# Optimization experiments

Hardware: AMD Instinct MI355X
Metric: run time of the kernel (lower is better)

The kernel has to match this reference:

```python
import jax, jax.numpy as jnp
import numpy as np
import math

B, NT, NS, NPS, D, H = 32, 64, 256, 256, 768, 12
DH = D // H
KEEP_RATIO = 0.7
LENS_KEEP = math.ceil(KEEP_RATIO * NS)  # 180
EPS = 1e-5


def _ln(z, g, b):
    m = jnp.mean(z, axis=-1, keepdims=True)
    v = jnp.mean((z - m) ** 2, axis=-1, keepdims=True)
    return (z - m) * jax.lax.rsqrt(v + EPS) * g + b


def setup_inputs() -> dict:
    key = jax.random.key(0)
    ks = jax.random.split(key, 12)
    p = lambda i, shape: jax.random.normal(ks[i], shape, jnp.float32) * 0.02
    return {
        'x': jax.random.normal(ks[0], (B, NT + NS, D), jnp.float32),
        'ps': jax.random.normal(ks[1], (B, NPS, D), jnp.float32),
        'global_index_template': jnp.broadcast_to(jnp.arange(NT, dtype=jnp.int32), (B, NT)),
        'global_index_search': jnp.broadcast_to(jnp.arange(NS, dtype=jnp.int32), (B, NS)),
        'g1': jnp.ones((D,), jnp.float32), 'b1': jnp.zeros((D,), jnp.float32),
        'Wqkv': p(2, (D, 3 * D)),
        'Wproj': p(3, (D, D)), 'bproj': jnp.zeros((D,), jnp.float32),
        'gt': jnp.ones((D,), jnp.float32), 'bt': jnp.zeros((D,), jnp.float32),
        'Wq': p(4, (D, D)), 'Wk': p(5, (D, D)), 'Wv': p(6, (D, D)),
        'Wtp': p(7, (D, D)), 'btp': jnp.zeros((D,), jnp.float32),
        'g2': jnp.ones((D,), jnp.float32), 'b2': jnp.zeros((D,), jnp.float32),
        'W1': p(8, (D, 4 * D)), 'b1m': jnp.zeros((4 * D,), jnp.float32),
        'W2': p(9, (4 * D, D)), 'b2m': jnp.zeros((D,), jnp.float32),
    }


def reference(x, ps, global_index_template, global_index_search,
              g1, b1, Wqkv, Wproj, bproj, gt, bt, Wq, Wk, Wv, Wtp, btp,
              g2, b2, W1, b1m, W2, b2m):
    scale = DH ** -0.5
    N = NT + NS
    # --- self attention over [template; search] tokens, raw attn exposed ---
    h = _ln(x, g1, b1)
    qkv = (h @ Wqkv).reshape(B, N, 3, H, DH)
    q = qkv[:, :, 0].transpose(0, 2, 1, 3)  # [B,H,N,DH]
    k = qkv[:, :, 1].transpose(0, 2, 1, 3)
    v = qkv[:, :, 2].transpose(0, 2, 1, 3)
    attn = jax.nn.softmax(jnp.einsum('bhqd,bhkd->bhqk', q, k) * scale, axis=-1)
    xa = jnp.einsum('bhqk,bhkd->bqhd', attn, v).reshape(B, N, D)
    x = x + xa @ Wproj + bproj

    # --- candidate elimination: keep top LENS_KEEP search tokens by
    # template->search attention averaged over heads and template queries ---
    attn_t = attn[:, :, :NT, NT:].mean(axis=(1, 2))  # [B, NS]
    order = jnp.argsort(-attn_t, axis=1)             # descending
    topk_idx = order[:, :LENS_KEEP]
    non_topk_idx = order[:, LENS_KEEP:]
    keep_index = jnp.take_along_axis(global_index_search, topk_idx, axis=1)
    removed_index = jnp.take_along_axis(global_index_search, non_topk_idx, axis=1)
    tokens_s = jnp.take_along_axis(x[:, NT:], topk_idx[:, :, None], axis=1)  # [B,LENS_KEEP,D]
    x = jnp.concatenate([x[:, :NT], tokens_s], axis=1)  # [B, NT+LENS_KEEP, D]

    # --- temporal cross-attention: kept search tokens attend over ps ---
    s = x[:, NT:]
    sn = _ln(s, gt, bt)
    qT = (sn @ Wq).reshape(B, LENS_KEEP, H, DH).transpose(0, 2, 1, 3)
    kT = (ps @ Wk).reshape(B, NPS, H, DH).transpose(0, 2, 1, 3)
    vT = (ps @ Wv).reshape(B, NPS, H, DH).transpose(0, 2, 1, 3)
    attn2 = jax.nn.softmax(jnp.einsum('bhqd,bhkd->bhqk', qT, kT) * scale, axis=-1)
    sa = jnp.einsum('bhqk,bhkd->bqhd', attn2, vT).reshape(B, LENS_KEEP, D)
    s = s + sa @ Wtp + btp
    x = jnp.concatenate([x[:, :NT], s], axis=1)

    # --- MLP (exact GELU like torch default) ---
    h2 = _ln(x, g2, b2)
    x = x + jax.nn.gelu(h2 @ W1 + b1m, approximate=False) @ W2 + b2m

    return (x, global_index_template, keep_index, removed_index, attn)
```

## Files before the change

### kernel.cpp

```cpp
#include <hip/hip_runtime.h>
#include <hip/hip_bf16.h>

#define BB 32
#define NT 64
#define NS 256
#define NN 320
#define NPS 256
#define DD 768
#define HH 12
#define DHD 64
#define LK 180
#define NREM 76

#define OFF_HF    0LL
#define OFF_KF    7864320LL
#define OFF_QTF   15728640LL
#define OFF_QV    17301504LL
#define OFF_WQVT  25165824LL
#define OFF_XA    0LL
#define OFF_X1    12000000LL
#define OFF_X2    0LL
#define OFF_SN    6000000LL
#define OFF_QT2   20000000LL
#define OFF_KT    22300000LL
#define OFF_VT    25500000LL
#define OFF_SA    6000000LL
#define OFF_H2    12000000LL
#define OFF_MIDB  15000000LL
#define OFF_WTS2  29300000LL
#define OFF_ATP   30500000LL
#define OFF_TOPK  30600000LL
#define OFF_WSM   30700000LL

#define O_X    0LL
#define O_GIT  5996544LL
#define O_KEEP 5998592LL
#define O_REM  6004352LL
#define O_ATTN 6006784LL

typedef __attribute__((ext_vector_type(8))) short short8v;
typedef __attribute__((ext_vector_type(4))) float f32x4;

__device__ __forceinline__ float bf2f(unsigned short u) {
  return __uint_as_float((unsigned)u << 16);
}
__device__ __forceinline__ unsigned short f2bfu(float f) {
  __hip_bfloat16 h = __float2bfloat16(f);
  return *reinterpret_cast<unsigned short*>(&h);
}

template<int OMODE>
__global__ __launch_bounds__(256) void ln_kernel(
    const float* __restrict__ in, float* __restrict__ outf,
    unsigned short* __restrict__ outh,
    const float* __restrict__ g, const float* __restrict__ b,
    int rpb, long long bstride, int row0)
{
  int r = blockIdx.x, t = threadIdx.x;
  long long base = (long long)(r / rpb) * bstride + (long long)(r % rpb + row0) * DD;
  float v0 = in[base + t], v1 = in[base + 256 + t], v2 = in[base + 512 + t];
  __shared__ float red[256];
  red[t] = v0 + v1 + v2;
  __syncthreads();
  #pragma unroll
  for (int off = 128; off > 0; off >>= 1) { if (t < off) red[t] += red[t + off]; __syncthreads(); }
  float mean = red[0] * (1.f / 768.f);
  __syncthreads();
  float d0 = v0 - mean, d1 = v1 - mean, d2 = v2 - mean;
  red[t] = d0 * d0 + d1 * d1 + d2 * d2;
  __syncthreads();
  #pragma unroll
  for (int off = 128; off > 0; off >>= 1) { if (t < off) red[t] += red[t + off]; __syncthreads(); }
  float rstd = rsqrtf(red[0] * (1.f / 768.f) + 1e-5f);
  long long ob = (long long)r * DD;
  float o0 = d0 * rstd * g[t]       + b[t];
  float o1 = d1 * rstd * g[256 + t] + b[256 + t];
  float o2 = d2 * rstd * g[512 + t] + b[512 + t];
  if (OMODE == 0) {
    outf[ob + t] = o0; outf[ob + 256 + t] = o1; outf[ob + 512 + t] = o2;
  } else {
    outh[ob + t] = f2bfu(o0); outh[ob + 256 + t] = f2bfu(o1); outh[ob + 512 + t] = f2bfu(o2);
  }
}

__global__ __launch_bounds__(256) void cvt_wt(
    const float* __restrict__ W, unsigned short* __restrict__ Th,
    int K, int Nfull, int n0off, int zoff, long long zdststep)
{
  __shared__ float tile[32][33];
  int z = blockIdx.z;
  unsigned short* T = Th + (long long)z * zdststep;
  int ncol = n0off + z * zoff;
  int n0 = blockIdx.x * 32, k0 = blockIdx.y * 32;
  int tx = threadIdx.x & 31, ty4 = (threadIdx.x >> 5) * 4;
  #pragma unroll
  for (int i = 0; i < 4; ++i)
    tile[ty4 + i][tx] = W[(long long)(k0 + ty4 + i) * Nfull + ncol + n0 + tx];
  __syncthreads();
  #pragma unroll
  for (int i = 0; i < 4; ++i)
    T[(long long)(n0 + ty4 + i) * K + k0 + tx] = f2bfu(tile[tx][ty4 + i]);
}

__global__ __launch_bounds__(256) void cvt_w5(
    const float* __restrict__ Wa, const float* __restrict__ Wb,
    const float* __restrict__ Wc, const float* __restrict__ Wd,
    const float* __restrict__ We, unsigned short* __restrict__ Th)
{
  __shared__ float tile[32][33];
  const float* srcs[5] = {Wa, Wb, Wc, Wd, We};
  const float* W = srcs[blockIdx.z];
  unsigned short* T = Th + (long long)blockIdx.z * (768 * 768);
  int n0 = blockIdx.x * 32, k0 = blockIdx.y * 32;
  int tx = threadIdx.x & 31, ty4 = (threadIdx.x >> 5) * 4;
  #pragma unroll
  for (int i = 0; i < 4; ++i)
    tile[ty4 + i][tx] = W[(long long)(k0 + ty4 + i) * 768 + n0 + tx];
  __syncthreads();
  #pragma unroll
  for (int i = 0; i < 4; ++i)
    T[(long long)(n0 + ty4 + i) * 768 + k0 + tx] = f2bfu(tile[tx][ty4 + i]);
}

__global__ __launch_bounds__(512) void gemm_k(
    const float* __restrict__ A, int a_rpb, long long a_bstride,
    const float* __restrict__ W, int wst,
    float* __restrict__ Cf, int c_ld, int M, int K)
{
  __shared__ float As[16][132];
  __shared__ float Ws[16][132];
  int t = threadIdx.x;
  long long bm = (long long)blockIdx.y * 128;
  long long bn = (long long)blockIdx.x * 128;
  float acc[4][8] = {};
  int wid = t >> 6, lane = t & 63;
  int tm = (wid & 3) * 32 + (lane >> 3) * 4;
  int tn = (wid >> 2) * 64 + (lane & 7) * 8;
  int idx = t << 2;
  int am = idx >> 4, ak = idx & 15;
  int wk = idx >> 7, wn2 = idx & 127;
  long long r = bm + am;
  long long abase = (r / a_rpb) * a_bstride + (r % a_rpb) * (long long)K;
  for (int k0 = 0; k0 < K; k0 += 16) {
    const float4 a4 = *reinterpret_cast<const float4*>(A + abase + k0 + ak);
    As[ak + 0][am] = a4.x; As[ak + 1][am] = a4.y;
    As[ak + 2][am] = a4.z; As[ak + 3][am] = a4.w;
    *reinterpret_cast<float4*>(&Ws[wk][wn2]) =
        *reinterpret_cast<const float4*>(W + (long long)(k0 + wk) * wst + bn + wn2);
    __syncthreads();
    #pragma unroll
    for (int kk = 0; kk < 16; ++kk) {
      float a[4], w[8];
      *reinterpret_cast<float4*>(a)     = *reinterpret_cast<const float4*>(&As[kk][tm]);
      *reinterpret_cast<float4*>(w)     = *reinterpret_cast<const float4*>(&Ws[kk][tn]);
      *reinterpret_cast<float4*>(w + 4) = *reinterpret_cast<const float4*>(&Ws[kk][tn + 4]);
      #pragma unroll
      for (int i = 0; i < 4; ++i)
        #pragma unroll
        for (int j = 0; j < 8; ++j)
          acc[i][j] = fmaf(a[i], w[j], acc[i][j]);
    }
    __syncthreads();
  }
  #pragma unroll
  for (int i = 0; i < 4; ++i) {
    long long crow = (bm + tm + i) * c_ld;
    #pragma unroll
    for (int j = 0; j < 8; ++j)
      Cf[crow + bn + tn + j] = acc[i][j];
  }
}

template<int AF32>
__global__ __launch_bounds__(256) void gemm_mfma(
    const void* __restrict__ A, const unsigned short* __restrict__ Bt,
    const float* __restrict__ bias, const float* __restrict__ resid,
    float* __restrict__ Cf, int ldf,
    unsigned short* __restrict__ Cb, int ldb, int colsplit,
    int M, int N, int K,
    int c_rpb, long long c_bstride, int c_row0, int act)
{
  __shared__ unsigned short As[128 * 40], Bs[128 * 40];
  const unsigned short* Ab = (const unsigned short*)A;
  const float* Af = (const float*)A;
  int t = threadIdx.x;
  long long bm = (long long)blockIdx.y * 128;
  long long bn = (long long)blockIdx.x * 128;
  int wid = t >> 6, lane = t & 63;
  int wr = (wid >> 1) << 6, wc = (wid & 1) << 6;
  f32x4 acc[4][4];
  #pragma unroll
  for (int m = 0; m < 4; ++m)
    #pragma unroll
    for (int n = 0; n < 4; ++n) acc[m][n] = (f32x4){0.f, 0.f, 0.f, 0.f};
  for (int k0 = 0; k0 < K; k0 += 32) {
    #pragma unroll
    for (int l = 0; l < 2; ++l) {
      int e = (t + (l << 8)) << 3;
      int row = e >> 5, kk = e & 31;
      int ls = row * 40 + kk;
      if (AF32) {
        const float4 f0 = *reinterpret_cast<const float4*>(&Af[(bm + row) * K + k0 + kk]);
        const float4 f1 = *reinterpret_cast<const float4*>(&Af[(bm + row) * K + k0 + kk + 4]);
        ushort4 u0, u1;
        u0.x = f2bfu(f0.x); u0.y = f2bfu(f0.y); u0.z = f2bfu(f0.z); u0.w = f2bfu(f0.w);
        u1.x = f2bfu(f1.x); u1.y = f2bfu(f1.y); u1.z = f2bfu(f1.z); u1.w = f2bfu(f1.w);
        *reinterpret_cast<ushort4*>(&As[ls])     = u0;
        *reinterpret_cast<ushort4*>(&As[ls + 4]) = u1;
      } else {
        *reinterpret_cast<int4*>(&As[ls]) = *reinterpret_cast<const int4*>(&Ab[(bm + row) * K + k0 + kk]);
      }
      *reinterpret_cast<int4*>(&Bs[ls]) = *reinterpret_cast<const int4*>(&Bt[(bn + row) * K + k0 + kk]);
    }
    __syncthreads();
    int ra = (wr + (lane & 15)) * 40 + ((lane >> 4) << 3);
    int rb = (wc + (lane & 15)) * 40 + ((lane >> 4) << 3);
    short8v a[4], b[4];
    #pragma unroll
    for (int m = 0; m < 4; ++m) {
      a[m] = *reinterpret_cast<const short8v*>(&As[ra + m * 16 * 40]);
      b[m] = *reinterpret_cast<const short8v*>(&Bs[rb + m * 16 * 40]);
    }
    #pragma unroll
    for (int m = 0; m < 4; ++m)
      #pragma unroll
      for (int n = 0; n < 4; ++n)
        acc[m][n] = __builtin_amdgcn_mfma_f32_16x16x32_bf16(a[m], b[n], acc[m][n], 0, 0, 0);
    __syncthreads();
  }
  int ro = (lane >> 4) << 2, co = lane & 15;
  #pragma unroll
  for (int m = 0; m < 4; ++m) {
    #pragma unroll
    for (int j = 0; j < 4; ++j) {
      long long r = bm + wr + m * 16 + ro + j;
      long long base = (r / c_rpb) * c_bstride + (long long)((int)(r % c_rpb) + c_row0) * ldf;
      #pragma unroll
      for (int n = 0; n < 4; ++n) {
        long long c = bn + wc + n * 16 + co;
        float v = acc[m][n][j];
        if (bias) v += bias[c];
        if (act) v = 0.5f * v * (1.f + erff(v * 0.70710678118654752f));
        if (resid) v += resid[base + c];
        if (c < colsplit) Cf[base + c] = v;
        else Cb[r * ldb + (c - colsplit)] = f2bfu(v);
      }
    }
  }
}

template<int NKV, int NW, int PROBS, int KF32>
__global__ __launch_bounds__(NW * 64) void attn_mfma(
    const unsigned short* __restrict__ q, int q_rs, int q_bs, int q_off,
    const void* __restrict__ kv, int k_rs,
    const unsigned short* __restrict__ v, int v_rs,
    unsigned short* __restrict__ xab, int xa_rs, int xa_bs, int xa_off,
    float* __restrict__ probs, int NQtot)
{
  constexpr int KST = 68;
  constexpr int VST = NKV + 4;
  constexpr int NT_K = NKV / 16;
  constexpr int NTH = NW * 64;
  __shared__ unsigned short ksh[NKV * KST];
  __shared__ unsigned short qsh[NW * 16 * KST];
  __shared__ unsigned short vsh[64 * VST];
  __shared__ float ldsT[PROBS ? NW * 16 * 17 : 1];
  int bh = blockIdx.x, b = bh / HH, h = bh % HH;
  int rb = blockIdx.y * (NW * 16);
  int t = threadIdx.x;
  const float* kf = (const float*)kv;
  const unsigned short* ku = (const unsigned short*)kv;
  for (int i = t; i < NKV * 64; i += NTH) {
    int kr = i >> 6, d = i & 63;
    long long gi = (long long)(b * NKV + kr);
    ksh[kr * KST + d] = KF32 ? f2bfu(kf[gi * k_rs + h * DHD + d])
                             : ku[gi * k_rs + h * DHD + d];
    int kp = (kr & ~31) | (((kr >> 2) & 3) << 3) | (((kr >> 4) & 1) << 2) | (kr & 3);
    vsh[d * VST + kp] = v[gi * v_rs + h * DHD + d];
  }
  for (int i = t; i < NW * 16 * 64; i += NTH) {
    int qr = i >> 6, d = i & 63;
    int qg = rb + qr;
    qsh[qr * KST + d] = (qg < NQtot)
      ? q[(long long)(b * q_bs + q_off + qg) * q_rs + h * DHD + d] : (unsigned short)0;
  }
  __syncthreads();
  int wid = t >> 6, lane = t & 63;
  int l15 = lane & 15, lg = lane >> 4;
  short8v bq[2];
  #pragma unroll
  for (int ks = 0; ks < 2; ++ks)
    bq[ks] = *reinterpret_cast<const short8v*>(&qsh[(wid * 16 + l15) * KST + ks * 32 + lg * 8]);
  f32x4 s[NT_K];
  #pragma unroll
  for (int mt = 0; mt < NT_K; ++mt) s[mt] = (f32x4){0.f, 0.f, 0.f, 0.f};
  #pragma unroll
  for (int mt = 0; mt < NT_K; ++mt)
    #pragma unroll
    for (int ks = 0; ks < 2; ++ks) {
      short8v ka = *reinterpret_cast<const short8v*>(&ksh[(mt * 16 + l15) * KST + ks * 32 + lg * 8]);
      s[mt] = __builtin_amdgcn_mfma_f32_16x16x32_bf16(ka, bq[ks], s[mt], 0, 0, 0);
    }
  float m = -3.4e38f;
  #pragma unroll
  for (int mt = 0; mt < NT_K; ++mt)
    #pragma unroll
    for (int j = 0; j < 4; ++j) { s[mt][j] *= 0.125f; m = fmaxf(m, s[mt][j]); }
  m = fmaxf(m, __shfl_xor(m, 16)); m = fmaxf(m, __shfl_xor(m, 32));
  float ss = 0.f;
  #pragma unroll
  for (int mt = 0; mt < NT_K; ++mt)
    #pragma unroll
    for (int j = 0; j < 4; ++j) { s[mt][j] = __expf(s[mt][j] - m); ss += s[mt][j]; }
  ss += __shfl_xor(ss, 16); ss += __shfl_xor(ss, 32);
  float inv = 1.f / ss;
  #pragma unroll
  for (int mt = 0; mt < NT_K; ++mt)
    #pragma unroll
    for (int j = 0; j < 4; ++j) s[mt][j] *= inv;
  if (PROBS) {
    float* lT = &ldsT[wid * 16 * 17];
    #pragma unroll
    for (int mt = 0; mt < NT_K; ++mt) {
      #pragma unroll
      for (int j = 0; j < 4; ++j) lT[l15 * 17 + lg * 4 + j] = s[mt][j];
      #pragma unroll
      for (int m4 = 0; m4 < 4; ++m4) {
        int qg = rb + wid * 16 + m4 * 4 + lg;
        if (qg < NQtot)
          probs[((long long)(bh * q_bs + q_off + qg)) * NKV + mt * 16 + l15] =
              lT[(m4 * 4 + lg) * 17 + l15];
      }
    }
  }
  f32x4 o[4];
  #pragma unroll
  for (int nt = 0; nt < 4; ++nt) o[nt] = (f32x4){0.f, 0.f, 0.f, 0.f};
  #pragma unroll
  for (int c = 0; c < NKV / 32; ++c) {
    short8v a8;
    #pragma unroll
    for (int j = 0; j < 4; ++j) {
      a8[j]     = (short)f2bfu(s[2 * c][j]);
      a8[4 + j] = (short)f2bfu(s[2 * c + 1][j]);
    }
    #pragma unroll
    for (int nt = 0; nt < 4; ++nt) {
      short8v bv = *reinterpret_cast<const short8v*>(&vsh[(nt * 16 + l15) * VST + c * 32 + lg * 8]);
      o[nt] = __builtin_amdgcn_mfma_f32_16x16x32_bf16(a8, bv, o[nt], 0, 0, 0);
    }
  }
  #pragma unroll
  for (int nt = 0; nt < 4; ++nt)
    #pragma unroll
    for (int j = 0; j < 4; ++j) {
      int qg = rb + wid * 16 + lg * 4 + j;
      if (qg < NQtot)
        xab[(long long)(b * xa_bs + xa_off + qg) * xa_rs + h * DHD + nt * 16 + l15] =
            f2bfu(o[nt][j]);
    }
}

__global__ __launch_bounds__(1024) void attn_tmpl(
    const float* __restrict__ qt, const float* __restrict__ kf,
    const unsigned short* __restrict__ vb,
    unsigned short* __restrict__ xab, float* __restrict__ probs,
    float* __restrict__ atp)
{
  constexpr int VST = NN + 4;
  __shared__ float ksh[NN * 65];
  __shared__ unsigned short vsh[64 * VST];
  __shared__ float pss[16][NN];
  __shared__ float qsh[16][64];
  int bh = blockIdx.x, b = bh / HH, h = bh % HH;
  int t = threadIdx.x;
  for (int i = t; i < NN * 64; i += 1024) {
    int rr = i >> 6, d = i & 63;
    long long gi = (long long)(b * NN + rr);
    ksh[rr * 65 + d] = kf[gi * 768 + h * DHD + d];
    vsh[d * VST + rr] = vb[gi * 1536 + h * DHD + d];
  }
  __syncthreads();
  int wid = t >> 6, lane = t & 63;
  float at[4] = {};
  for (int q = wid; q < NT; q += 16) {
    qsh[wid][lane] = qt[(long long)(b * NT + q) * 768 + h * DHD + lane];
    float s[5];
    #pragma unroll
    for (int r = 0; r < 5; ++r) s[r] = 0.f;
    const float* kp = ksh + lane * 65;
    #pragma unroll 16
    for (int d = 0; d < 64; ++d) {
      float qd = qsh[wid][d];
      #pragma unroll
      for (int r = 0; r < 5; ++r)
        s[r] = fmaf(qd, kp[(r << 6) * 65 + d], s[r]);
    }
    float m = -3.4e38f;
    #pragma unroll
    for (int r = 0; r < 5; ++r) { s[r] *= 0.125f; m = fmaxf(m, s[r]); }
    #pragma unroll
    for (int off = 32; off > 0; off >>= 1) m = fmaxf(m, __shfl_xor(m, off));
    float ss = 0.f;
    #pragma unroll
    for (int r = 0; r < 5; ++r) { s[r] = __expf(s[r] - m); ss += s[r]; }
    #pragma unroll
    for (int off = 32; off > 0; off >>= 1) ss += __shfl_xor(ss, off);
    float inv = 1.f / ss;
    long long pb = ((long long)(bh * NN) + q) * NN;
    #pragma unroll
    for (int r = 0; r < 5; ++r) {
      float p = s[r] * inv;
      s[r] = p;
      pss[wid][lane + (r << 6)] = p;
      probs[pb + lane + (r << 6)] = p;
    }
    #pragma unroll
    for (int r = 1; r < 5; ++r) at[r - 1] += s[r];
    float acc = 0.f;
    const unsigned short* vp = vsh + lane * VST;
    #pragma unroll 8
    for (int j = 0; j < NN; j += 4) {
      float4 p4 = *reinterpret_cast<const float4*>(&pss[wid][j]);
      ushort4 v4 = *reinterpret_cast<const ushort4*>(&vp[j]);
      acc = fmaf(p4.x, bf2f(v4.x), acc);
      acc = fmaf(p4.y, bf2f(v4.y), acc);
      acc = fmaf(p4.z, bf2f(v4.z), acc);
      acc = fmaf(p4.w, bf2f(v4.w), acc);
    }
    xab[(long long)(b * NN + q) * 768 + h * DHD + lane] = f2bfu(acc);
  }
  #pragma unroll
  for (int r = 1; r < 5; ++r) pss[wid][lane + ((r - 1) << 6)] = at[r - 1];
  __syncthreads();
  if (t < 256) {
    float v = 0.f;
    #pragma unroll
    for (int w = 0; w < 16; ++w) v += pss[w][t];
    atp[(long long)bh * 256 + t] = v;
  }
}

__global__ __launch_bounds__(256) void sort_kernel(
    const float* __restrict__ atp, const int* __restrict__ gis,
    float* __restrict__ keep_out, float* __restrict__ rem_out,
    int* __restrict__ topk)
{
  int b = blockIdx.x, t = threadIdx.x;
  __shared__ float sv[256];
  __shared__ int   si[256];
  float v = 0.f;
  for (int h = 0; h < HH; ++h) v += atp[((long long)(b * HH + h) << 8) + t];
  sv[t] = v; si[t] = t;
  __syncthreads();
  for (int k = 2; k <= 256; k <<= 1) {
    for (int j = k >> 1; j > 0; j >>= 1) {
      int ixj = t ^ j;
      if (ixj > t) {
        float va = sv[t], vb2 = sv[ixj];
        int ia = si[t], ib = si[ixj];
        bool after = (va < vb2) || (va == vb2 && ia > ib);
        bool dirUp = ((t & k) == 0);
        if (after == dirUp) { sv[t] = vb2; sv[ixj] = va; si[t] = ib; si[ixj] = ia; }
      }
      __syncthreads();
    }
  }
  int o = si[t];
  if (t < LK) {
    topk[b * LK + t] = o;
    keep_out[b * LK + t] = (float)gis[(b << 8) + o];
  } else {
    rem_out[b * NREM + (t - LK)] = (float)gis[(b << 8) + o];
  }
}

__global__ __launch_bounds__(256) void gather_kernel(
    const float* __restrict__ x1, const int* __restrict__ topk, float* __restrict__ x2)
{
  int r = blockIdx.x, t = threadIdx.x;
  int b = r / 244, rr = r % 244;
  int src = (rr < NT) ? rr : (NT + topk[b * LK + (rr - NT)]);
  const float* s = x1 + (long long)(b * NN + src) * DD;
  float* d = x2 + (long long)r * DD;
  d[t] = s[t]; d[256 + t] = s[256 + t]; d[512 + t] = s[512 + t];
}

__global__ void git_kernel(const int* __restrict__ git, float* __restrict__ o)
{
  int i = blockIdx.x * 256 + threadIdx.x;
  if (i < BB * NT) o[i] = (float)git[i];
}

extern "C" void kernel_launch(void* const* d_in, const int* in_sizes, int n_in,
                              void* d_out, int out_size, void* d_ws, size_t ws_size,
                              hipStream_t stream) {
  (void)in_sizes; (void)n_in; (void)out_size; (void)ws_size;
  const float* x    = (const float*)d_in[0];
  const float* ps   = (const float*)d_in[1];
  const int*   git  = (const int*)d_in[2];
  const int*   gis  = (const int*)d_in[3];
  const float* g1   = (const float*)d_in[4];
  const float* b1   = (const float*)d_in[5];
  const float* Wqkv = (const float*)d_in[6];
  const float* Wproj= (const float*)d_in[7];
  const float* bproj= (const float*)d_in[8];
  const float* gt   = (const float*)d_in[9];
  const float* bt   = (const float*)d_in[10];
  const float* Wq   = (const float*)d_in[11];
  const float* Wk   = (const float*)d_in[12];
  const float* Wv   = (const float*)d_in[13];
  const float* Wtp  = (const float*)d_in[14];
  const float* btp  = (const float*)d_in[15];
  const float* g2   = (const float*)d_in[16];
  const float* b2   = (const float*)d_in[17];
  const float* W1   = (const float*)d_in[18];
  const float* b1m  = (const float*)d_in[19];
  const float* W2   = (const float*)d_in[20];
  const float* b2m  = (const float*)d_in[21];
  float* wsf = (float*)d_ws;
  float* out = (float*)d_out;
  unsigned short* WQVT = (unsigned short*)(wsf + OFF_WQVT);
  unsigned short* QVp  = (unsigned short*)(wsf + OFF_QV);
  unsigned short* XAp  = (unsigned short*)(wsf + OFF_XA);
  unsigned short* WSMp = (unsigned short*)(wsf + OFF_WSM);
  unsigned short* WTS2 = (unsigned short*)(wsf + OFF_WTS2);
  unsigned short* SNp  = (unsigned short*)(wsf + OFF_SN);
  unsigned short* QT2p = (unsigned short*)(wsf + OFF_QT2);
  unsigned short* KTp  = (unsigned short*)(wsf + OFF_KT);
  unsigned short* VTp  = (unsigned short*)(wsf + OFF_VT);
  unsigned short* SAp  = (unsigned short*)(wsf + OFF_SA);
  unsigned short* H2p  = (unsigned short*)(wsf + OFF_H2);
  unsigned short* MIDp = (unsigned short*)(wsf + OFF_MIDB);
  #define WSLOT(i) (WSMp + (long long)(i) * 768 * 768)

  hipLaunchKernelGGL(cvt_wt, dim3(24, 24, 2), dim3(256), 0, stream,
                     Wqkv, WQVT, DD, 3 * DD, 0, 1536, (long long)768 * 768);
  hipLaunchKernelGGL(cvt_w5, dim3(24, 24, 5), dim3(256), 0, stream,
                     Wproj, Wq, Wk, Wv, Wtp, WSMp);
  hipLaunchKernelGGL((ln_kernel<0>), dim3(BB * NN), dim3(256), 0, stream,
                     x, wsf + OFF_HF, (unsigned short*)nullptr, g1, b1, BB * NN, 0LL, 0);
  hipLaunchKernelGGL(gemm_k, dim3(6, 80), dim3(512), 0, stream,
                     wsf + OFF_HF, BB * NN, 0LL, Wqkv + 768, 3 * DD,
                     wsf + OFF_KF, DD, BB * NN, DD);
  hipLaunchKernelGGL(gemm_k, dim3(6, 16), dim3(512), 0, stream,
                     wsf + OFF_HF, NT, (long long)NN * DD, Wqkv, 3 * DD,
                     wsf + OFF_QTF, DD, BB * NT, DD);
  hipLaunchKernelGGL((gemm_mfma<1>), dim3(12, 80), dim3(256), 0, stream,
                     (const void*)(wsf + OFF_HF), WQVT,
                     (const float*)nullptr, (const float*)nullptr,
                     (float*)nullptr, 1, QVp, 1536, 0,
                     BB * NN, 1536, DD, BB * NN, 0LL, 0, 0);
  hipLaunchKernelGGL((attn_mfma<NN, 8, 1, 1>), dim3(BB * HH, 2), dim3(512), 0, stream,
                     QVp, 1536, NN, NT,
                     (const void*)(wsf + OFF_KF), DD,
                     QVp + 768, 1536,
                     XAp, DD, NN, NT,
                     out + O_ATTN, 256);
  hipLaunchKernelGGL(attn_tmpl, dim3(BB * HH), dim3(1024), 0, stream,
                     wsf + OFF_QTF, wsf + OFF_KF, QVp + 768,
                     XAp, out + O_ATTN, wsf + OFF_ATP);
  hipLaunchKernelGGL((gemm_mfma<0>), dim3(6, 80), dim3(256), 0, stream,
                     (const void*)XAp, WSLOT(0), bproj, x,
                     wsf + OFF_X1, DD, (unsigned short*)nullptr, 1, DD,
                     BB * NN, DD, DD, BB * NN, 0LL, 0, 0);
  hipLaunchKernelGGL(sort_kernel, dim3(BB), dim3(256), 0, stream,
                     wsf + OFF_ATP, gis, out + O_KEEP, out + O_REM,
                     (int*)(wsf + OFF_TOPK));
  hipLaunchKernelGGL(git_kernel, dim3((BB * NT + 255) / 256), dim3(256), 0, stream,
                     git, out + O_GIT);
  hipLaunchKernelGGL(gather_kernel, dim3(BB * 244), dim3(256), 0, stream,
                     wsf + OFF_X1, (const int*)(wsf + OFF_TOPK), wsf + OFF_X2);
  hipLaunchKernelGGL((ln_kernel<1>), dim3(BB * LK), dim3(256), 0, stream,
                     wsf + OFF_X2, (float*)nullptr, SNp, gt, bt, LK, (long long)244 * DD, NT);
  hipLaunchKernelGGL((gemm_mfma<0>), dim3(6, 45), dim3(256), 0, stream,
                     (const void*)SNp, WSLOT(1), (const float*)nullptr, (const float*)nullptr,
                     (float*)nullptr, 1, QT2p, DD, 0,
                     BB * LK, DD, DD, BB * LK, 0LL, 0, 0);
  hipLaunchKernelGGL((gemm_mfma<1>), dim3(6, 64), dim3(256), 0, stream,
                     (const void*)ps, WSLOT(2), (const float*)nullptr, (const float*)nullptr,
                     (float*)nullptr, 1, KTp, DD, 0,
                     BB * NPS, DD, DD, BB * NPS, 0LL, 0, 0);
  hipLaunchKernelGGL((gemm_mfma<1>), dim3(6, 64), dim3(256), 0, stream,
                     (const void*)ps, WSLOT(3), (const float*)nullptr, (const float*)nullptr,
                     (float*)nullptr, 1, VTp, DD, 0,
                     BB * NPS, DD, DD, BB * NPS, 0LL, 0, 0);
  hipLaunchKernelGGL((attn_mfma<NPS, 8, 0, 0>), dim3(BB * HH, 2), dim3(512), 0, stream,
                     QT2p, DD, LK, 0,
                     (const void*)KTp, DD,
                     VTp, DD,
                     SAp, DD, LK, 0,
                     (float*)nullptr, LK);
  hipLaunchKernelGGL((gemm_mfma<0>), dim3(6, 45), dim3(256), 0, stream,
                     (const void*)SAp, WSLOT(4), btp, wsf + OFF_X2,
                     wsf + OFF_X2, DD, (unsigned short*)nullptr, 1, DD,
                     BB * LK, DD, DD, LK, (long long)244 * DD, NT, 0);
  hipLaunchKernelGGL((ln_kernel<1>), dim3(BB * 244), dim3(256), 0, stream,
                     wsf + OFF_X2, (float*)nullptr, H2p, g2, b2, BB * 244, 0LL, 0);
  hipLaunchKernelGGL(cvt_wt, dim3(96, 24, 1), dim3(256), 0, stream,
                     W1, WTS2, DD, 4 * DD, 0, 0, 0LL);
  hipLaunchKernelGGL((gemm_mfma<0>), dim3(24, 61), dim3(256), 0, stream,
                     (const void*)H2p, WTS2, b1m, (const float*)nullptr,
                     (float*)nullptr, 1, MIDp, 4 * DD, 0,
                     BB * 244, 4 * DD, DD, BB * 244, 0LL, 0, 1);
  hipLaunchKernelGGL(cvt_wt, dim3(24, 96, 1), dim3(256), 0, stream,
                     W2, WTS2, 4 * DD, DD, 0, 0, 0LL);
  hipLaunchKernelGGL((gemm_mfma<0>), dim3(6, 61), dim3(256), 0, stream,
                     (const void*)MIDp, WTS2, b2m, wsf + OFF_X2,
                     out + O_X, DD, (unsigned short*)nullptr, 1, DD,
                     BB * 244, DD, 4 * DD, BB * 244, 0LL, 0, 0);
}
```

Baseline: 1.078 ms.

## Use direct global-to-LDS loads in MFMA GEMM with bf16-only A inputs

The MFMA GEMM now stages A and B tiles with global_load_lds (16-byte direct-to-LDS loads) into an unpadded 32-wide LDS layout, replacing register round-trips. The fp32-A template path is removed: LayerNorm now also writes a bf16 copy of its output, and ps is converted to bf16 once by a new kernel, so the K/V projections no longer convert per tile. The fp32 SIMT gemm_k also gains register prefetch of the next K slice. Unpadded LDS rows may add bank conflicts on the fragment reads, and the extra conversion kernel and bf16 buffers add memory traffic and workspace reuse risk.

Measured after the change: 1.035 ms, median of 2. -4.0%, faster.

```diff
diff --git a/kernel.cpp b/kernel.cpp
--- a/kernel.cpp
+++ b/kernel.cpp
@@ -17,13 +17,15 @@
 #define OFF_QTF   15728640LL
 #define OFF_QV    17301504LL
 #define OFF_WQVT  25165824LL
+#define OFF_HB    26000000LL
 #define OFF_XA    0LL
 #define OFF_X1    12000000LL
 #define OFF_X2    0LL
 #define OFF_SN    6000000LL
-#define OFF_QT2   20000000LL
-#define OFF_KT    22300000LL
-#define OFF_VT    25500000LL
+#define OFF_PSB   17301504LL
+#define OFF_QT2   20500000LL
+#define OFF_KT    22800000LL
+#define OFF_VT    26000000LL
 #define OFF_SA    6000000LL
 #define OFF_H2    12000000LL
 #define OFF_MIDB  15000000LL
@@ -48,6 +50,11 @@
   __hip_bfloat16 h = __float2bfloat16(f);
   return *reinterpret_cast<unsigned short*>(&h);
 }
+__device__ __forceinline__ void gload16(const unsigned short* g, unsigned short* l) {
+  __builtin_amdgcn_global_load_lds(
+      (const __attribute__((address_space(1))) unsigned int*)g,
+      (__attribute__((address_space(3))) unsigned int*)l, 16, 0, 0);
+}
 
 template<int OMODE>
 __global__ __launch_bounds__(256) void ln_kernel(
@@ -76,9 +83,10 @@
   float o0 = d0 * rstd * g[t]       + b[t];
   float o1 = d1 * rstd * g[256 + t] + b[256 + t];
   float o2 = d2 * rstd * g[512 + t] + b[512 + t];
-  if (OMODE == 0) {
+  if (OMODE == 0 || OMODE == 3) {
     outf[ob + t] = o0; outf[ob + 256 + t] = o1; outf[ob + 512 + t] = o2;
-  } else {
+  }
+  if (OMODE == 1 || OMODE == 3) {
     outh[ob + t] = f2bfu(o0); outh[ob + 256 + t] = f2bfu(o1); outh[ob + 512 + t] = f2bfu(o2);
   }
 }
@@ -120,6 +128,18 @@
   #pragma unroll
   for (int i = 0; i < 4; ++i)
     T[(long long)(n0 + ty4 + i) * 768 + k0 + tx] = f2bfu(tile[tx][ty4 + i]);
+}
+
+__global__ __launch_bounds__(256) void cvt_bf_kernel(
+    const float* __restrict__ in, unsigned short* __restrict__ out, long long n)
+{
+  long long i = ((long long)blockIdx.x * 256 + threadIdx.x) * 4;
+  if (i < n) {
+    float4 v = *reinterpret_cast<const float4*>(&in[i]);
+    ushort4 o;
+    o.x = f2bfu(v.x); o.y = f2bfu(v.y); o.z = f2bfu(v.z); o.w = f2bfu(v.w);
+    *reinterpret_cast<ushort4*>(&out[i]) = o;
+  }
 }
 
 __global__ __launch_bounds__(512) void gemm_k(
@@ -141,13 +161,17 @@
   int wk = idx >> 7, wn2 = idx & 127;
   long long r = bm + am;
   long long abase = (r / a_rpb) * a_bstride + (r % a_rpb) * (long long)K;
+  float4 a4 = *reinterpret_cast<const float4*>(A + abase + ak);
+  float4 w4 = *reinterpret_cast<const float4*>(W + (long long)wk * wst + bn + wn2);
   for (int k0 = 0; k0 < K; k0 += 16) {
-    const float4 a4 = *reinterpret_cast<const float4*>(A + abase + k0 + ak);
     As[ak + 0][am] = a4.x; As[ak + 1][am] = a4.y;
     As[ak + 2][am] = a4.z; As[ak + 3][am] = a4.w;
-    *reinterpret_cast<float4*>(&Ws[wk][wn2]) =
-        *reinterpret_cast<const float4*>(W + (long long)(k0 + wk) * wst + bn + wn2);
+    *reinterpret_cast<float4*>(&Ws[wk][wn2]) = w4;
     __syncthreads();
+    if (k0 + 16 < K) {
+      a4 = *reinterpret_cast<const float4*>(A + abase + k0 + 16 + ak);
+      w4 = *reinterpret_cast<const float4*>(W + (long long)(k0 + 16 + wk) * wst + bn + wn2);
+    }
     #pragma unroll
     for (int kk = 0; kk < 16; ++kk) {
       float a[4], w[8];
@@ -171,55 +195,50 @@
   }
 }
 
-template<int AF32>
 __global__ __launch_bounds__(256) void gemm_mfma(
-    const void* __restrict__ A, const unsigned short* __restrict__ Bt,
+    const unsigned short* __restrict__ A, const unsigned short* __restrict__ Bt,
     const float* __restrict__ bias, const float* __restrict__ resid,
     float* __restrict__ Cf, int ldf,
     unsigned short* __restrict__ Cb, int ldb, int colsplit,
     int M, int N, int K,
     int c_rpb, long long c_bstride, int c_row0, int act)
 {
-  __shared__ unsigned short As[128 * 40], Bs[128 * 40];
-  const unsigned short* Ab = (const unsigned short*)A;
-  const float* Af = (const float*)A;
+  __shared__ unsigned short As[128 * 32], Bs[128 * 32];
   int t = threadIdx.x;
   long long bm = (long long)blockIdx.y * 128;
   long long bn = (long long)blockIdx.x * 128;
   int wid = t >> 6, lane = t & 63;
   int wr = (wid >> 1) << 6, wc = (wid & 1) << 6;
+  int e0 = (wid << 9) + lane * 8;
+  int e1 = ((4 + wid) << 9) + lane * 8;
+  int r0 = e0 >> 5, c0 = e0 & 31;
+  int r1 = e1 >> 5, c1 = e1 & 31;
+  unsigned short* As0 = &As[(long long)(wid << 9)];
+  unsigned short* As1 = &As[(long long)((4 + wid) << 9)];
+  unsigned short* Bs0 = &Bs[(long long)(wid << 9)];
+  unsigned short* Bs1 = &Bs[(long long)((4 + wid) << 9)];
+  const unsigned short* Ar0 = A + (bm + r0) * (long long)K + c0;
+  const unsigned short* Ar1 = A + (bm + r1) * (long long)K + c1;
+  const unsigned short* Br0 = Bt + (bn + r0) * (long long)K + c0;
+  const unsigned short* Br1 = Bt + (bn + r1) * (long long)K + c1;
   f32x4 acc[4][4];
   #pragma unroll
   for (int m = 0; m < 4; ++m)
     #pragma unroll
     for (int n = 0; n < 4; ++n) acc[m][n] = (f32x4){0.f, 0.f, 0.f, 0.f};
+  int ra = (wr + (lane & 15)) * 32 + ((lane >> 4) << 3);
+  int rb = (wc + (lane & 15)) * 32 + ((lane >> 4) << 3);
   for (int k0 = 0; k0 < K; k0 += 32) {
-    #pragma unroll
-    for (int l = 0; l < 2; ++l) {
-      int e = (t + (l << 8)) << 3;
-      int row = e >> 5, kk = e & 31;
-      int ls = row * 40 + kk;
-      if (AF32) {
-        const float4 f0 = *reinterpret_cast<const float4*>(&Af[(bm + row) * K + k0 + kk]);
-        const float4 f1 = *reinterpret_cast<const float4*>(&Af[(bm + row) * K + k0 + kk + 4]);
-        ushort4 u0, u1;
-        u0.x = f2bfu(f0.x); u0.y = f2bfu(f0.y); u0.z = f2bfu(f0.z); u0.w = f2bfu(f0.w);
-        u1.x = f2bfu(f1.x); u1.y = f2bfu(f1.y); u1.z = f2bfu(f1.z); u1.w = f2bfu(f1.w);
-        *reinterpret_cast<ushort4*>(&As[ls])     = u0;
-        *reinterpret_cast<ushort4*>(&As[ls + 4]) = u1;
-      } else {
-        *reinterpret_cast<int4*>(&As[ls]) = *reinterpret_cast<const int4*>(&Ab[(bm + row) * K + k0 + kk]);
-      }
-      *reinterpret_cast<int4*>(&Bs[ls]) = *reinterpret_cast<const int4*>(&Bt[(bn + row) * K + k0 + kk]);
-    }
+    gload16(Ar0 + k0, As0);
+    gload16(Ar1 + k0, As1);
+    gload16(Br0 + k0, Bs0);
+    gload16(Br1 + k0, Bs1);
     __syncthreads();
-    int ra = (wr + (lane & 15)) * 40 + ((lane >> 4) << 3);
-    int rb = (wc + (lane & 15)) * 40 + ((lane >> 4) << 3);
     short8v a[4], b[4];
     #pragma unroll
     for (int m = 0; m < 4; ++m) {
-      a[m] = *reinterpret_cast<const short8v*>(&As[ra + m * 16 * 40]);
-      b[m] = *reinterpret_cast<const short8v*>(&Bs[rb + m * 16 * 40]);
+      a[m] = *reinterpret_cast<const short8v*>(&As[ra + m * 512]);
+      b[m] = *reinterpret_cast<const short8v*>(&Bs[rb + m * 512]);
     }
     #pragma unroll
     for (int m = 0; m < 4; ++m)
@@ -521,11 +540,13 @@
   float* wsf = (float*)d_ws;
   float* out = (float*)d_out;
   unsigned short* WQVT = (unsigned short*)(wsf + OFF_WQVT);
+  unsigned short* HBp  = (unsigned short*)(wsf + OFF_HB);
   unsigned short* QVp  = (unsigned short*)(wsf + OFF_QV);
   unsigned short* XAp  = (unsigned short*)(wsf + OFF_XA);
   unsigned short* WSMp = (unsigned short*)(wsf + OFF_WSM);
   unsigned short* WTS2 = (unsigned short*)(wsf + OFF_WTS2);
   unsigned short* SNp  = (unsigned short*)(wsf + OFF_SN);
+  unsigned short* PSBp = (unsigned short*)(wsf + OFF_PSB);
   unsigned short* QT2p = (unsigned short*)(wsf + OFF_QT2);
   unsigned short* KTp  = (unsigned short*)(wsf + OFF_KT);
   unsigned short* VTp  = (unsigned short*)(wsf + OFF_VT);
@@ -538,17 +559,16 @@
                      Wqkv, WQVT, DD, 3 * DD, 0, 1536, (long long)768 * 768);
   hipLaunchKernelGGL(cvt_w5, dim3(24, 24, 5), dim3(256), 0, stream,
                      Wproj, Wq, Wk, Wv, Wtp, WSMp);
-  hipLaunchKernelGGL((ln_kernel<0>), dim3(BB * NN), dim3(256), 0, stream,
-                     x, wsf + OFF_HF, (unsigned short*)nullptr, g1, b1, BB * NN, 0LL, 0);
+  hipLaunchKernelGGL((ln_kernel<3>), dim3(BB * NN), dim3(256), 0, stream,
+                     x, wsf + OFF_HF, HBp, g1, b1, BB * NN, 0LL, 0);
   hipLaunchKernelGGL(gemm_k, dim3(6, 80), dim3(512), 0, stream,
                      wsf + OFF_HF, BB * NN, 0LL, Wqkv + 768, 3 * DD,
                      wsf + OFF_KF, DD, BB * NN, DD);
   hipLaunchKernelGGL(gemm_k, dim3(6, 16), dim3(512), 0, stream,
                      wsf + OFF_HF, NT, (long long)NN * DD, Wqkv, 3 * DD,
                      wsf + OFF_QTF, DD, BB * NT, DD);
-  hipLaunchKernelGGL((gemm_mfma<1>), dim3(12, 80), dim3(256), 0, stream,
-                     (const void*)(wsf + OFF_HF), WQVT,
-                     (const float*)nullptr, (const float*)nullptr,
+  hipLaunchKernelGGL(gemm_mfma, dim3(12, 80), dim3(256), 0, stream,
+                     HBp, WQVT, (const float*)nullptr, (const float*)nullptr,
                      (float*)nullptr, 1, QVp, 1536, 0,
                      BB * NN, 1536, DD, BB * NN, 0LL, 0, 0);
   hipLaunchKernelGGL((attn_mfma<NN, 8, 1, 1>), dim3(BB * HH, 2), dim3(512), 0, stream,
@@ -560,8 +580,8 @@
   hipLaunchKernelGGL(attn_tmpl, dim3(BB * HH), dim3(1024), 0, stream,
                      wsf + OFF_QTF, wsf + OFF_KF, QVp + 768,
                      XAp, out + O_ATTN, wsf + OFF_ATP);
-  hipLaunchKernelGGL((gemm_mfma<0>), dim3(6, 80), dim3(256), 0, stream,
-                     (const void*)XAp, WSLOT(0), bproj, x,
+  hipLaunchKernelGGL(gemm_mfma, dim3(6, 80), dim3(256), 0, stream,
+                     XAp, WSLOT(0), bproj, x,
                      wsf + OFF_X1, DD, (unsigned short*)nullptr, 1, DD,
                      BB * NN, DD, DD, BB * NN, 0LL, 0, 0);
   hipLaunchKernelGGL(sort_kernel, dim3(BB), dim3(256), 0, stream,
@@ -571,18 +591,20 @@
                      git, out + O_GIT);
   hipLaunchKernelGGL(gather_kernel, dim3(BB * 244), dim3(256), 0, stream,
                      wsf + OFF_X1, (const int*)(wsf + OFF_TOPK), wsf + OFF_X2);
+  hipLaunchKernelGGL(cvt_bf_kernel, dim3(6144), dim3(256), 0, stream,
+                     ps, PSBp, (long long)BB * NPS * DD);
   hipLaunchKernelGGL((ln_kernel<1>), dim3(BB * LK), dim3(256), 0, stream,
                      wsf + OFF_X2, (float*)nullptr, SNp, gt, bt, LK, (long long)244 * DD, NT);
-  hipLaunchKernelGGL((gemm_mfma<0>), dim3(6, 45), dim3(256), 0, stream,
-                     (const void*)SNp, WSLOT(1), (const float*)nullptr, (const float*)nullptr,
+  hipLaunchKernelGGL(gemm_mfma, dim3(6, 45), dim3(256), 0, stream,
+                     SNp, WSLOT(1), (const float*)nullptr, (const float*)nullptr,
                      (float*)nullptr, 1, QT2p, DD, 0,
                      BB * LK, DD, DD, BB * LK, 0LL, 0, 0);
-  hipLaunchKernelGGL((gemm_mfma<1>), dim3(6, 64), dim3(256), 0, stream,
-                     (const void*)ps, WSLOT(2), (const float*)nullptr, (const float*)nullptr,
+  hipLaunchKernelGGL(gemm_mfma, dim3(6, 64), dim3(256), 0, stream,
+                     PSBp, WSLOT(2), (const float*)nullptr, (const float*)nullptr,
                      (float*)nullptr, 1, KTp, DD, 0,
                      BB * NPS, DD, DD, BB * NPS, 0LL, 0, 0);
-  hipLaunchKernelGGL((gemm_mfma<1>), dim3(6, 64), dim3(256), 0, stream,
-                     (const void*)ps, WSLOT(3), (const float*)nullptr, (const float*)nullptr,
+  hipLaunchKernelGGL(gemm_mfma, dim3(6, 64), dim3(256), 0, stream,
+                     PSBp, WSLOT(3), (const float*)nullptr, (const float*)nullptr,
                      (float*)nullptr, 1, VTp, DD, 0,
                      BB * NPS, DD, DD, BB * NPS, 0LL, 0, 0);
   hipLaunchKernelGGL((attn_mfma<NPS, 8, 0, 0>), dim3(BB * HH, 2), dim3(512), 0, stream,
@@ -591,22 +613,22 @@
                      VTp, DD,
                      SAp, DD, LK, 0,
                      (float*)nullptr, LK);
-  hipLaunchKernelGGL((gemm_mfma<0>), dim3(6, 45), dim3(256), 0, stream,
-                     (const void*)SAp, WSLOT(4), btp, wsf + OFF_X2,
+  hipLaunchKernelGGL(gemm_mfma, dim3(6, 45), dim3(256), 0, stream,
+                     SAp, WSLOT(4), btp, wsf + OFF_X2,
                      wsf + OFF_X2, DD, (unsigned short*)nullptr, 1, DD,
                      BB * LK, DD, DD, LK, (long long)244 * DD, NT, 0);
   hipLaunchKernelGGL((ln_kernel<1>), dim3(BB * 244), dim3(256), 0, stream,
                      wsf + OFF_X2, (float*)nullptr, H2p, g2, b2, BB * 244, 0LL, 0);
   hipLaunchKernelGGL(cvt_wt, dim3(96, 24, 1), dim3(256), 0, stream,
                      W1, WTS2, DD, 4 * DD, 0, 0, 0LL);
-  hipLaunchKernelGGL((gemm_mfma<0>), dim3(24, 61), dim3(256), 0, stream,
-                     (const void*)H2p, WTS2, b1m, (const float*)nullptr,
+  hipLaunchKernelGGL(gemm_mfma, dim3(24, 61), dim3(256), 0, stream,
+                     H2p, WTS2, b1m, (const float*)nullptr,
                      (float*)nullptr, 1, MIDp, 4 * DD, 0,
                      BB * 244, 4 * DD, DD, BB * 244, 0LL, 0, 1);
   hipLaunchKernelGGL(cvt_wt, dim3(24, 96, 1), dim3(256), 0, stream,
                      W2, WTS2, 4 * DD, DD, 0, 0, 0LL);
-  hipLaunchKernelGGL((gemm_mfma<0>), dim3(6, 61), dim3(256), 0, stream,
-                     (const void*)MIDp, WTS2, b2m, wsf + OFF_X2,
+  hipLaunchKernelGGL(gemm_mfma, dim3(6, 61), dim3(256), 0, stream,
+                     MIDp, WTS2, b2m, wsf + OFF_X2,
                      out + O_X, DD, (unsigned short*)nullptr, 1, DD,
                      BB * 244, DD, 4 * DD, BB * 244, 0LL, 0, 0);
 }
```
